# Kernel tuning notes

Hardware: AMD Instinct MI355X
Metric: run time of the kernel (lower is better)

Reference implementation:

```python
import jax, jax.numpy as jnp
import numpy as np

N_NODES = 16384
HID_IN = 1024   # hid_size (GCN in/out dim)
HID_MID = 1500  # hidden_size
N_EDGES = 131072


def setup_inputs() -> dict:
    key = jax.random.key(0)
    k1, k2, k3, k4, k5, k6 = jax.random.split(key, 6)
    x = jax.random.normal(k1, (N_NODES, HID_IN), dtype=jnp.float32)
    edge_index = jax.random.randint(k2, (2, N_EDGES), 0, N_NODES, dtype=jnp.int64)
    # GCNConv weights (glorot-ish scale) and biases
    W1 = jax.random.normal(k3, (HID_IN, HID_MID), dtype=jnp.float32) / np.sqrt(HID_IN)
    b1 = jnp.zeros((HID_MID,), dtype=jnp.float32)
    W2 = jax.random.normal(k4, (HID_MID, HID_IN), dtype=jnp.float32) / np.sqrt(HID_MID)
    b2 = jnp.zeros((HID_IN,), dtype=jnp.float32)
    return {"x": x, "edge_index": edge_index, "W1": W1, "b1": b1, "W2": W2, "b2": b2}


def _gcn_conv(x, W, b, src, dst, inv_sqrt_deg, n_nodes):
    # PyG GCNConv: out[i] = sum_{(j->i)} d_j^{-1/2} d_i^{-1/2} (x W)[j] + b
    h = x @ W                                   # [N, out]
    norm = inv_sqrt_deg[src] * inv_sqrt_deg[dst]  # [E]
    msg = h[src] * norm[:, None]                 # gather + scale [E, out]
    out = jax.ops.segment_sum(msg, dst, num_segments=n_nodes)
    return out + b


def reference(x, edge_index, W1, b1, W2, b2):
    n = x.shape[0]
    # add self-loops (GCNConv default)
    loops = jnp.arange(n, dtype=edge_index.dtype)
    src = jnp.concatenate([edge_index[0], loops])
    dst = jnp.concatenate([edge_index[1], loops])
    deg = jax.ops.segment_sum(jnp.ones_like(dst, dtype=x.dtype), dst, num_segments=n)
    inv_sqrt_deg = jnp.where(deg > 0, jax.lax.rsqrt(jnp.maximum(deg, 1.0)), 0.0)
    h = _gcn_conv(x, W1, b1, src, dst, inv_sqrt_deg, n)
    h = jax.nn.relu(h)  # dropout skipped (eval mode)
    out = _gcn_conv(h, W2, b2, src, dst, inv_sqrt_deg, n)
    return out
```

## Files before the change

kernel.cpp:

```cpp
#include <hip/hip_runtime.h>
#include <cstdint>
#include <cstddef>

#define NN 16384
#define DIN 1024
#define DMID 1500
#define DMIDP 1536
#define NE 131072

typedef __bf16 bf16;
typedef __bf16 bf16x4 __attribute__((ext_vector_type(4)));
typedef __bf16 bf16x8 __attribute__((ext_vector_type(8)));
typedef float f32x4 __attribute__((ext_vector_type(4)));

#define GLOBAL_AS __attribute__((address_space(1)))
#define LDS_AS __attribute__((address_space(3)))

__device__ __forceinline__ void gload_lds16(const bf16* g, bf16* l) {
    __builtin_amdgcn_global_load_lds((GLOBAL_AS const unsigned int*)(g),
                                     (LDS_AS unsigned int*)(l), 16, 0, 0);
}

#define SBAR() asm volatile("s_barrier" ::: "memory")
#define WAITV_(N) asm volatile("s_waitcnt vmcnt(" #N ")" ::: "memory")
#define WAITV(N) WAITV_(N)
#define WAITL0() asm volatile("s_waitcnt lgkmcnt(0)" ::: "memory")

__global__ void k_zero_cnt(int* cnt) {
    cnt[blockIdx.x * 256 + threadIdx.x] = 0;
}

__global__ void k_count(const int* __restrict__ dst, int* cnt) {
    int e = blockIdx.x * 256 + threadIdx.x;
    atomicAdd(&cnt[dst[e]], 1);
}

__global__ __launch_bounds__(1024) void k_scan(const int* __restrict__ cnt,
                                               int* __restrict__ rowptr,
                                               int* __restrict__ cursor,
                                               float* __restrict__ isd) {
    __shared__ int sums[1024];
    int t = threadIdx.x;
    int base = t * 16;
    int v[16], p[16];
    int s = 0;
#pragma unroll
    for (int k = 0; k < 16; ++k) {
        v[k] = cnt[base + k];
        p[k] = (v[k] + 7) & ~7;
        s += p[k];
    }
    sums[t] = s;
    __syncthreads();
    for (int off = 1; off < 1024; off <<= 1) {
        int y = (t >= off) ? sums[t - off] : 0;
        __syncthreads();
        sums[t] += y;
        __syncthreads();
    }
    int run = sums[t] - s;
#pragma unroll
    for (int k = 0; k < 16; ++k) {
        rowptr[base + k] = run;
        cursor[base + k] = run;
        isd[base + k] = rsqrtf((float)(v[k] + 1));
        run += p[k];
    }
    if (t == 1023) rowptr[NN] = run;
}

__global__ void k_fill(const int* __restrict__ src, const int* __restrict__ dst,
                       int* cursor, const float* __restrict__ isd,
                       int* __restrict__ csr_src, float* __restrict__ csr_w) {
    int e = blockIdx.x * 256 + threadIdx.x;
    int s = src[e], d = dst[e];
    int pos = atomicAdd(&cursor[d], 1);
    csr_src[pos] = s;
    csr_w[pos] = isd[s] * isd[d];
}

__global__ void k_pad(const int* __restrict__ cnt, const int* __restrict__ rowptr,
                      int* __restrict__ csr_src, float* __restrict__ csr_w) {
    int i = blockIdx.x * 256 + threadIdx.x;
    int c = cnt[i];
    int p = (c + 7) & ~7;
    int base = rowptr[i];
    for (int q = c; q < p; ++q) {
        csr_src[base + q] = i;
        csr_w[base + q] = 0.0f;
    }
}

__global__ void k_cvt_x(const float4* __restrict__ x, bf16x4* __restrict__ xb) {
    int i = blockIdx.x * 256 + threadIdx.x;
    float4 v = x[i];
    bf16x4 o;
    o[0] = (bf16)v.x; o[1] = (bf16)v.y; o[2] = (bf16)v.z; o[3] = (bf16)v.w;
    xb[i] = o;
}

__global__ void k_cvt_w1(const float* __restrict__ W1, bf16* __restrict__ W1b) {
    int n = blockIdx.x;
    for (int k = threadIdx.x; k < DIN; k += 256)
        W1b[n * DIN + k] = (n < DMID) ? (bf16)W1[(size_t)k * DMID + n] : (bf16)0.0f;
}

__global__ void k_cvt_w2(const float* __restrict__ W2, bf16* __restrict__ W2b) {
    int n = blockIdx.x;
    for (int k = threadIdx.x; k < DMIDP; k += 256)
        W2b[n * DMIDP + k] = (k < DMID) ? (bf16)W2[(size_t)k * DIN + n] : (bf16)0.0f;
}

template <int K, int N, bool RELU_BIAS>
__global__ __launch_bounds__(512, 2) void gemm256(const bf16* __restrict__ A,
                                                  const bf16* __restrict__ Bt,
                                                  bf16* __restrict__ C,
                                                  const float* __restrict__ bias) {
    constexpr int NT = K / 64;
    __shared__ __align__(16) bf16 lds[2][2][256 * 64];
    const int tid = threadIdx.x;
    const int w = tid >> 6;
    const int lane = tid & 63;
    const int bm = blockIdx.x, bn = blockIdx.y;
    const int fr = lane & 15, fq = lane >> 4;
    const int wm = w >> 2;
    const int wn = w & 3;
    const int sx = fr & 7;

    const int lrow = lane >> 3;
    const int lslot = (lane & 7) ^ lrow;
    const bf16* gA = A + (size_t)(bm * 256 + w * 8 + lrow) * K + lslot * 8;
    const bf16* gB = Bt + (size_t)(bn * 256 + w * 8 + lrow) * K + lslot * 8;
    bf16* lA0 = &lds[0][0][0] + w * 512;
    bf16* lB0 = &lds[0][1][0] + w * 512;
    bf16* lA1 = &lds[1][0][0] + w * 512;
    bf16* lB1 = &lds[1][1][0] + w * 512;

    f32x4 acc[8][4];
#pragma unroll
    for (int i = 0; i < 8; ++i)
#pragma unroll
        for (int j = 0; j < 4; ++j) acc[i][j] = {0.f, 0.f, 0.f, 0.f};

#define STAGE(T, LA, LB)                                                  \
    do {                                                                  \
        const bf16* _ga = gA + (size_t)(T) * 64;                          \
        const bf16* _gb = gB + (size_t)(T) * 64;                          \
        _Pragma("unroll") for (int r = 0; r < 4; ++r)                     \
            gload_lds16(_ga + (size_t)r * (64 * K), (LA) + r * 4096);     \
        _Pragma("unroll") for (int r = 0; r < 4; ++r)                     \
            gload_lds16(_gb + (size_t)r * (64 * K), (LB) + r * 4096);     \
    } while (0)

#define LDA4(BUF, MH, KS)                                                             \
    _Pragma("unroll") for (int mt = 0; mt < 4; ++mt) {                                \
        int row = wm * 128 + (MH) * 64 + mt * 16 + fr;                                \
        int sl = (((KS) << 2) | fq) ^ sx;                                             \
        af[mt] = *(const bf16x8*)((const char*)&lds[BUF][0][0] + row * 128 + sl * 16);\
    }
#define LDB4(BUF, KS)                                                                 \
    _Pragma("unroll") for (int nt = 0; nt < 4; ++nt) {                                \
        int row = wn * 64 + nt * 16 + fr;                                             \
        int sl = (((KS) << 2) | fq) ^ sx;                                             \
        bq[nt] = *(const bf16x8*)((const char*)&lds[BUF][1][0] + row * 128 + sl * 16);\
    }
#define MFMA16(MH)                                                                    \
    _Pragma("unroll") for (int mt = 0; mt < 4; ++mt)                                  \
    _Pragma("unroll") for (int nt = 0; nt < 4; ++nt)                                  \
        acc[(MH) * 4 + mt][nt] = __builtin_amdgcn_mfma_f32_16x16x32_bf16(             \
            af[mt], bq[nt], acc[(MH) * 4 + mt][nt], 0, 0, 0);

    STAGE(0, lA0, lB0);
    STAGE(1, lA1, lB1);
    WAITV(8);
    SBAR();

#pragma unroll 2
    for (int t = 0; t < NT; ++t) {
        const int b = t & 1;
        bf16x8 af[4], bq[4];
        LDB4(b, 0); LDA4(b, 0, 0);
        SBAR(); WAITL0();
        __builtin_amdgcn_s_setprio(1); MFMA16(0); __builtin_amdgcn_s_setprio(0);
        SBAR();
        LDA4(b, 1, 0);
        SBAR(); WAITL0();
        __builtin_amdgcn_s_setprio(1); MFMA16(1); __builtin_amdgcn_s_setprio(0);
        SBAR();
        LDB4(b, 1); LDA4(b, 0, 1);
        SBAR(); WAITL0();
        __builtin_amdgcn_s_setprio(1); MFMA16(0); __builtin_amdgcn_s_setprio(0);
        SBAR();
        LDA4(b, 1, 1);
        SBAR(); WAITL0();
        __builtin_amdgcn_s_setprio(1); MFMA16(1); __builtin_amdgcn_s_setprio(0);
        SBAR();
        if (t + 2 < NT) {
            if (b == 0) { STAGE(t + 2, lA0, lB0); } else { STAGE(t + 2, lA1, lB1); }
            WAITV(8);
            SBAR();
        } else if (t + 1 < NT) {
            WAITV(0);
            SBAR();
        }
    }
#undef STAGE
#undef LDA4
#undef LDB4
#undef MFMA16

    float bv[4];
    if (RELU_BIAS) {
#pragma unroll
        for (int nt = 0; nt < 4; ++nt) {
            int col = bn * 256 + wn * 64 + nt * 16 + fr;
            bv[nt] = (col < DMID) ? bias[col] : 0.0f;
        }
    }
#pragma unroll
    for (int mq = 0; mq < 8; ++mq) {
        int row0 = bm * 256 + wm * 128 + mq * 16 + fq * 4;
#pragma unroll
        for (int nt = 0; nt < 4; ++nt) {
            int col = bn * 256 + wn * 64 + nt * 16 + fr;
#pragma unroll
            for (int r = 0; r < 4; ++r) {
                float v = acc[mq][nt][r];
                if (RELU_BIAS) v = fmaxf(v + bv[nt], 0.0f);
                C[(size_t)(row0 + r) * N + col] = (bf16)v;
            }
        }
    }
}

__global__ __launch_bounds__(128) void k_aggX(const bf16* __restrict__ X,
                                              const int* __restrict__ rowptr,
                                              const int* __restrict__ csr_src,
                                              const float* __restrict__ csr_w,
                                              const float* __restrict__ isd,
                                              bf16* __restrict__ XA) {
    int i = blockIdx.x;
    int t = threadIdx.x;
    int c0 = t * 8;
    int beg = rowptr[i], end = rowptr[i + 1];
    float wi = isd[i];
    float w0 = wi * wi;
    float a[8];
    bf16x8 h = *(const bf16x8*)&X[(size_t)i * DIN + c0];
#pragma unroll
    for (int k = 0; k < 8; ++k) a[k] = w0 * (float)h[k];
    for (int e = beg; e < end; e += 8) {
        int j[8];
        float w[8];
        bf16x8 hv[8];
#pragma unroll
        for (int q = 0; q < 8; ++q) { j[q] = csr_src[e + q]; w[q] = csr_w[e + q]; }
#pragma unroll
        for (int q = 0; q < 8; ++q)
            hv[q] = *(const bf16x8*)&X[(size_t)j[q] * DIN + c0];
#pragma unroll
        for (int q = 0; q < 8; ++q)
#pragma unroll
            for (int k = 0; k < 8; ++k) a[k] += w[q] * (float)hv[q][k];
    }
    bf16x8 o;
#pragma unroll
    for (int k = 0; k < 8; ++k) o[k] = (bf16)a[k];
    *(bf16x8*)&XA[(size_t)i * DIN + c0] = o;
}

__global__ __launch_bounds__(128) void k_agg2(const bf16* __restrict__ H,
                                              const int* __restrict__ rowptr,
                                              const int* __restrict__ csr_src,
                                              const float* __restrict__ csr_w,
                                              const float* __restrict__ isd,
                                              const float* __restrict__ b2,
                                              float* __restrict__ out) {
    int i = blockIdx.x;
    int t = threadIdx.x;
    int c0 = t * 8;
    int beg = rowptr[i], end = rowptr[i + 1];
    float wi = isd[i];
    float w0 = wi * wi;
    float a[8];
    bf16x8 h = *(const bf16x8*)&H[(size_t)i * DIN + c0];
#pragma unroll
    for (int k = 0; k < 8; ++k) a[k] = w0 * (float)h[k];
    for (int e = beg; e < end; e += 8) {
        int j[8];
        float w[8];
        bf16x8 hv[8];
#pragma unroll
        for (int q = 0; q < 8; ++q) { j[q] = csr_src[e + q]; w[q] = csr_w[e + q]; }
#pragma unroll
        for (int q = 0; q < 8; ++q)
            hv[q] = *(const bf16x8*)&H[(size_t)j[q] * DIN + c0];
#pragma unroll
        for (int q = 0; q < 8; ++q)
#pragma unroll
            for (int k = 0; k < 8; ++k) a[k] += w[q] * (float)hv[q][k];
    }
    float4 o0, o1;
    o0.x = a[0] + b2[c0 + 0]; o0.y = a[1] + b2[c0 + 1];
    o0.z = a[2] + b2[c0 + 2]; o0.w = a[3] + b2[c0 + 3];
    o1.x = a[4] + b2[c0 + 4]; o1.y = a[5] + b2[c0 + 5];
    o1.z = a[6] + b2[c0 + 6]; o1.w = a[7] + b2[c0 + 7];
    *(float4*)&out[(size_t)i * DIN + c0] = o0;
    *(float4*)&out[(size_t)i * DIN + c0 + 4] = o1;
}

extern "C" void kernel_launch(void* const* d_in, const int* in_sizes, int n_in,
                              void* d_out, int out_size, void* d_ws, size_t ws_size,
                              hipStream_t stream) {
    const float* x = (const float*)d_in[0];
    const int* ei = (const int*)d_in[1];
    const float* W1 = (const float*)d_in[2];
    const float* b1 = (const float*)d_in[3];
    const float* W2 = (const float*)d_in[4];
    const float* b2 = (const float*)d_in[5];
    float* out = (float*)d_out;
    const int* src = ei;
    const int* dst = ei + NE;

    char* ws = (char*)d_ws;
    int* cnt      = (int*)(ws + 0);
    int* cursor   = (int*)(ws + 65536);
    float* isd    = (float*)(ws + 131072);
    int* rowptr   = (int*)(ws + 196608);
    int* csr_src  = (int*)(ws + 327680);
    float* csr_w  = (float*)(ws + 2424832);
    bf16* Xb      = (bf16*)(ws + 4521984);
    bf16* XA      = (bf16*)(ws + 38076416);
    bf16* W1b     = (bf16*)(ws + 71630848);
    bf16* W2b     = (bf16*)(ws + 74776576);
    bf16* Y1b     = (bf16*)(ws + 77922304);
    bf16* H2b     = XA;

    k_zero_cnt<<<NN / 256, 256, 0, stream>>>(cnt);
    k_count<<<NE / 256, 256, 0, stream>>>(dst, cnt);
    k_scan<<<1, 1024, 0, stream>>>(cnt, rowptr, cursor, isd);
    k_fill<<<NE / 256, 256, 0, stream>>>(src, dst, cursor, isd, csr_src, csr_w);
    k_pad<<<NN / 256, 256, 0, stream>>>(cnt, rowptr, csr_src, csr_w);

    k_cvt_x<<<NN * DIN / 4 / 256, 256, 0, stream>>>((const float4*)x, (bf16x4*)Xb);
    k_cvt_w1<<<DMIDP, 256, 0, stream>>>(W1, W1b);
    k_cvt_w2<<<DIN, 256, 0, stream>>>(W2, W2b);

    k_aggX<<<NN, 128, 0, stream>>>(Xb, rowptr, csr_src, csr_w, isd, XA);
    dim3 g1(NN / 256, DMIDP / 256);
    gemm256<DIN, DMIDP, true><<<g1, 512, 0, stream>>>(XA, W1b, Y1b, b1);

    dim3 g2(NN / 256, DIN / 256);
    gemm256<DMIDP, DIN, false><<<g2, 512, 0, stream>>>(Y1b, W2b, H2b, nullptr);
    k_agg2<<<NN, 128, 0, stream>>>(H2b, rowptr, csr_src, csr_w, isd, b2, out);
}
```

Before: 398.2 us.

## Software-pipeline LDS fragment loads with register double buffering in GEMM loop

The GEMM main loop is restructured so LDS-to-register fragment loads for the next MFMA group are issued while the current MFMA group runs. It uses separate a0/a1/b0/b1 register sets, and the next tile's first fragments are prefetched right after the buffer-swap barrier. This drops most of the per-substep barriers and lgkmcnt waits that previously serialized LDS reads and MFMA work. In exchange it uses more VGPRs for fragment buffers and waits on global loads once per iteration. It also removes the unroll-2 pragma, so the buffer index becomes a runtime value.

```diff
diff --git a/kernel.cpp b/kernel.cpp
--- a/kernel.cpp
+++ b/kernel.cpp
@@ -131,10 +131,6 @@
     const int lslot = (lane & 7) ^ lrow;
     const bf16* gA = A + (size_t)(bm * 256 + w * 8 + lrow) * K + lslot * 8;
     const bf16* gB = Bt + (size_t)(bn * 256 + w * 8 + lrow) * K + lslot * 8;
-    bf16* lA0 = &lds[0][0][0] + w * 512;
-    bf16* lB0 = &lds[0][1][0] + w * 512;
-    bf16* lA1 = &lds[1][0][0] + w * 512;
-    bf16* lB1 = &lds[1][1][0] + w * 512;
 
     f32x4 acc[8][4];
 #pragma unroll
@@ -142,67 +138,67 @@
 #pragma unroll
         for (int j = 0; j < 4; ++j) acc[i][j] = {0.f, 0.f, 0.f, 0.f};
 
-#define STAGE(T, LA, LB)                                                  \
-    do {                                                                  \
-        const bf16* _ga = gA + (size_t)(T) * 64;                          \
-        const bf16* _gb = gB + (size_t)(T) * 64;                          \
-        _Pragma("unroll") for (int r = 0; r < 4; ++r)                     \
-            gload_lds16(_ga + (size_t)r * (64 * K), (LA) + r * 4096);     \
-        _Pragma("unroll") for (int r = 0; r < 4; ++r)                     \
-            gload_lds16(_gb + (size_t)r * (64 * K), (LB) + r * 4096);     \
+#define STAGE(T, BUF)                                                          \
+    do {                                                                       \
+        const bf16* _ga = gA + (size_t)(T) * 64;                               \
+        const bf16* _gb = gB + (size_t)(T) * 64;                               \
+        bf16* _la = &lds[BUF][0][0] + w * 512;                                 \
+        bf16* _lb = &lds[BUF][1][0] + w * 512;                                 \
+        _Pragma("unroll") for (int r = 0; r < 4; ++r)                          \
+            gload_lds16(_ga + (size_t)r * (64 * K), _la + r * 4096);           \
+        _Pragma("unroll") for (int r = 0; r < 4; ++r)                          \
+            gload_lds16(_gb + (size_t)r * (64 * K), _lb + r * 4096);           \
     } while (0)
 
-#define LDA4(BUF, MH, KS)                                                             \
-    _Pragma("unroll") for (int mt = 0; mt < 4; ++mt) {                                \
-        int row = wm * 128 + (MH) * 64 + mt * 16 + fr;                                \
-        int sl = (((KS) << 2) | fq) ^ sx;                                             \
-        af[mt] = *(const bf16x8*)((const char*)&lds[BUF][0][0] + row * 128 + sl * 16);\
-    }
-#define LDB4(BUF, KS)                                                                 \
-    _Pragma("unroll") for (int nt = 0; nt < 4; ++nt) {                                \
-        int row = wn * 64 + nt * 16 + fr;                                             \
-        int sl = (((KS) << 2) | fq) ^ sx;                                             \
-        bq[nt] = *(const bf16x8*)((const char*)&lds[BUF][1][0] + row * 128 + sl * 16);\
-    }
-#define MFMA16(MH)                                                                    \
-    _Pragma("unroll") for (int mt = 0; mt < 4; ++mt)                                  \
-    _Pragma("unroll") for (int nt = 0; nt < 4; ++nt)                                  \
-        acc[(MH) * 4 + mt][nt] = __builtin_amdgcn_mfma_f32_16x16x32_bf16(             \
-            af[mt], bq[nt], acc[(MH) * 4 + mt][nt], 0, 0, 0);
-
-    STAGE(0, lA0, lB0);
-    STAGE(1, lA1, lB1);
+#define LDA4(DST, BUF, MH, KS)                                                 \
+    _Pragma("unroll") for (int mt = 0; mt < 4; ++mt) {                         \
+        int row = wm * 128 + (MH) * 64 + mt * 16 + fr;                         \
+        int sl = (((KS) << 2) | fq) ^ sx;                                      \
+        DST[mt] = *(const bf16x8*)((const char*)&lds[BUF][0][0] +              \
+                                   row * 128 + sl * 16);                       \
+    }
+#define LDB4(DST, BUF, KS)                                                     \
+    _Pragma("unroll") for (int nt = 0; nt < 4; ++nt) {                         \
+        int row = wn * 64 + nt * 16 + fr;                                      \
+        int sl = (((KS) << 2) | fq) ^ sx;                                      \
+        DST[nt] = *(const bf16x8*)((const char*)&lds[BUF][1][0] +              \
+                                   row * 128 + sl * 16);                       \
+    }
+#define MFMA16(MH, AF, BF)                                                     \
+    __builtin_amdgcn_s_setprio(1);                                             \
+    _Pragma("unroll") for (int mt = 0; mt < 4; ++mt)                           \
+    _Pragma("unroll") for (int nt = 0; nt < 4; ++nt)                           \
+        acc[(MH) * 4 + mt][nt] = __builtin_amdgcn_mfma_f32_16x16x32_bf16(      \
+            AF[mt], BF[nt], acc[(MH) * 4 + mt][nt], 0, 0, 0);                  \
+    __builtin_amdgcn_s_setprio(0);
+
+    bf16x8 a0[4], a1[4], b0[4], b1[4];
+
+    STAGE(0, 0);
+    STAGE(1, 1);
     WAITV(8);
     SBAR();
-
-#pragma unroll 2
+    LDA4(a0, 0, 0, 0);
+    LDB4(b0, 0, 0);
+
     for (int t = 0; t < NT; ++t) {
         const int b = t & 1;
-        bf16x8 af[4], bq[4];
-        LDB4(b, 0); LDA4(b, 0, 0);
-        SBAR(); WAITL0();
-        __builtin_amdgcn_s_setprio(1); MFMA16(0); __builtin_amdgcn_s_setprio(0);
-        SBAR();
-        LDA4(b, 1, 0);
-        SBAR(); WAITL0();
-        __builtin_amdgcn_s_setprio(1); MFMA16(1); __builtin_amdgcn_s_setprio(0);
-        SBAR();
-        LDB4(b, 1); LDA4(b, 0, 1);
-        SBAR(); WAITL0();
-        __builtin_amdgcn_s_setprio(1); MFMA16(0); __builtin_amdgcn_s_setprio(0);
-        SBAR();
-        LDA4(b, 1, 1);
-        SBAR(); WAITL0();
-        __builtin_amdgcn_s_setprio(1); MFMA16(1); __builtin_amdgcn_s_setprio(0);
-        SBAR();
-        if (t + 2 < NT) {
-            if (b == 0) { STAGE(t + 2, lA0, lB0); } else { STAGE(t + 2, lA1, lB1); }
-            WAITV(8);
-            SBAR();
-        } else if (t + 1 < NT) {
+        LDA4(a1, b, 1, 0);
+        MFMA16(0, a0, b0);
+        LDA4(a0, b, 0, 1);
+        LDB4(b1, b, 1);
+        MFMA16(1, a1, b0);
+        LDA4(a1, b, 1, 1);
+        MFMA16(0, a0, b1);
+        if (t + 1 < NT) {
+            WAITL0();
             WAITV(0);
             SBAR();
+            if (t + 2 < NT) STAGE(t + 2, b);
+            LDA4(a0, b ^ 1, 0, 0);
+            LDB4(b0, b ^ 1, 0);
         }
+        MFMA16(1, a1, b1);
     }
 #undef STAGE
 #undef LDA4
```

Measured after the change: 378.1 us. -5.0%, faster.

## Interleave half-tile global-to-LDS staging with MFMA phases in GEMM main loop

Applied to the files above, without the earlier changes.

Restructures the GEMM main loop so each quarter-phase issues a half-tile of the next A/B stage while computing. A is prefetched one step ahead and B two steps ahead, instead of the whole next tile being staged at the loop end. Register fragments are reorganized so A rows are loaded once per K-half and reused across two B column halves, which cuts LDS reads. This raises register pressure and relies on a subtle buffer-reuse ordering between the A and B buffers.

```diff
diff --git a/kernel.cpp b/kernel.cpp
--- a/kernel.cpp
+++ b/kernel.cpp
@@ -129,12 +129,8 @@
 
     const int lrow = lane >> 3;
     const int lslot = (lane & 7) ^ lrow;
-    const bf16* gA = A + (size_t)(bm * 256 + w * 8 + lrow) * K + lslot * 8;
-    const bf16* gB = Bt + (size_t)(bn * 256 + w * 8 + lrow) * K + lslot * 8;
-    bf16* lA0 = &lds[0][0][0] + w * 512;
-    bf16* lB0 = &lds[0][1][0] + w * 512;
-    bf16* lA1 = &lds[1][0][0] + w * 512;
-    bf16* lB1 = &lds[1][1][0] + w * 512;
+    const bf16* gA = A + (size_t)(bm * 256 + lrow) * K + lslot * 8;
+    const bf16* gB = Bt + (size_t)(bn * 256 + lrow) * K + lslot * 8;
 
     f32x4 acc[8][4];
 #pragma unroll
@@ -142,70 +138,81 @@
 #pragma unroll
         for (int j = 0; j < 4; ++j) acc[i][j] = {0.f, 0.f, 0.f, 0.f};
 
-#define STAGE(T, LA, LB)                                                  \
-    do {                                                                  \
-        const bf16* _ga = gA + (size_t)(T) * 64;                          \
-        const bf16* _gb = gB + (size_t)(T) * 64;                          \
-        _Pragma("unroll") for (int r = 0; r < 4; ++r)                     \
-            gload_lds16(_ga + (size_t)r * (64 * K), (LA) + r * 4096);     \
-        _Pragma("unroll") for (int r = 0; r < 4; ++r)                     \
-            gload_lds16(_gb + (size_t)r * (64 * K), (LB) + r * 4096);     \
+#define STAGEH(T, BUF, MAT, HALF)                                              \
+    do {                                                                       \
+        const bf16* _g = (MAT) ? gB : gA;                                      \
+        bf16* _l = &lds[BUF][MAT][0] + ((HALF) * 128 + w * 16) * 64;           \
+        _Pragma("unroll") for (int r = 0; r < 2; ++r)                          \
+            gload_lds16(_g + (size_t)((HALF) * 128 + w * 16 + r * 8) * K       \
+                           + (size_t)(T) * 64,                                 \
+                        _l + r * 512);                                         \
     } while (0)
 
-#define LDA4(BUF, MH, KS)                                                             \
-    _Pragma("unroll") for (int mt = 0; mt < 4; ++mt) {                                \
-        int row = wm * 128 + (MH) * 64 + mt * 16 + fr;                                \
-        int sl = (((KS) << 2) | fq) ^ sx;                                             \
-        af[mt] = *(const bf16x8*)((const char*)&lds[BUF][0][0] + row * 128 + sl * 16);\
-    }
-#define LDB4(BUF, KS)                                                                 \
-    _Pragma("unroll") for (int nt = 0; nt < 4; ++nt) {                                \
-        int row = wn * 64 + nt * 16 + fr;                                             \
-        int sl = (((KS) << 2) | fq) ^ sx;                                             \
-        bq[nt] = *(const bf16x8*)((const char*)&lds[BUF][1][0] + row * 128 + sl * 16);\
-    }
-#define MFMA16(MH)                                                                    \
-    _Pragma("unroll") for (int mt = 0; mt < 4; ++mt)                                  \
-    _Pragma("unroll") for (int nt = 0; nt < 4; ++nt)                                  \
-        acc[(MH) * 4 + mt][nt] = __builtin_amdgcn_mfma_f32_16x16x32_bf16(             \
-            af[mt], bq[nt], acc[(MH) * 4 + mt][nt], 0, 0, 0);
-
-    STAGE(0, lA0, lB0);
-    STAGE(1, lA1, lB1);
-    WAITV(8);
+#define LDA8(DST, BUF, MH)                                                     \
+    _Pragma("unroll") for (int mt = 0; mt < 4; ++mt)                           \
+    _Pragma("unroll") for (int ks = 0; ks < 2; ++ks) {                         \
+        int row = wm * 128 + (MH) * 64 + mt * 16 + fr;                         \
+        int sl = ((ks << 2) | fq) ^ sx;                                        \
+        DST[mt][ks] = *(const bf16x8*)((const char*)&lds[BUF][0][0] +          \
+                                       row * 128 + sl * 16);                   \
+    }
+#define LDB4(DST, BUF, NH)                                                     \
+    _Pragma("unroll") for (int nt = 0; nt < 2; ++nt)                           \
+    _Pragma("unroll") for (int ks = 0; ks < 2; ++ks) {                         \
+        int row = wn * 64 + (NH) * 32 + nt * 16 + fr;                          \
+        int sl = ((ks << 2) | fq) ^ sx;                                        \
+        DST[nt][ks] = *(const bf16x8*)((const char*)&lds[BUF][1][0] +          \
+                                       row * 128 + sl * 16);                   \
+    }
+#define MFMA16(MH, NH, AF, BF)                                                 \
+    __builtin_amdgcn_s_setprio(1);                                             \
+    _Pragma("unroll") for (int mt = 0; mt < 4; ++mt)                           \
+    _Pragma("unroll") for (int nt = 0; nt < 2; ++nt)                           \
+    _Pragma("unroll") for (int ks = 0; ks < 2; ++ks)                           \
+        acc[(MH) * 4 + mt][(NH) * 2 + nt] =                                    \
+            __builtin_amdgcn_mfma_f32_16x16x32_bf16(                           \
+                AF[mt][ks], BF[nt][ks], acc[(MH) * 4 + mt][(NH) * 2 + nt],     \
+                0, 0, 0);                                                      \
+    __builtin_amdgcn_s_setprio(0);
+
+    STAGEH(0, 0, 0, 0); STAGEH(0, 0, 0, 1);
+    STAGEH(0, 0, 1, 0); STAGEH(0, 0, 1, 1);
+    STAGEH(1, 1, 1, 0); STAGEH(1, 1, 1, 1);
+    WAITV(4);
     SBAR();
 
+    bf16x8 a[4][2], b0[2][2], b1[2][2];
 #pragma unroll 2
     for (int t = 0; t < NT; ++t) {
-        const int b = t & 1;
-        bf16x8 af[4], bq[4];
-        LDB4(b, 0); LDA4(b, 0, 0);
+        const int c = t & 1;
+        LDA8(a, c, 0);
+        LDB4(b0, c, 0);
+        if (t + 1 < NT) STAGEH(t + 1, c ^ 1, 0, 0);
         SBAR(); WAITL0();
-        __builtin_amdgcn_s_setprio(1); MFMA16(0); __builtin_amdgcn_s_setprio(0);
-        SBAR();
-        LDA4(b, 1, 0);
+        MFMA16(0, 0, a, b0);
+        SBAR();
+        LDB4(b1, c, 1);
+        if (t + 1 < NT) STAGEH(t + 1, c ^ 1, 0, 1);
         SBAR(); WAITL0();
-        __builtin_amdgcn_s_setprio(1); MFMA16(1); __builtin_amdgcn_s_setprio(0);
-        SBAR();
-        LDB4(b, 1); LDA4(b, 0, 1);
+        MFMA16(0, 1, a, b1);
+        SBAR();
+        LDA8(a, c, 1);
+        if (t + 2 < NT) STAGEH(t + 2, c, 1, 0);
         SBAR(); WAITL0();
-        __builtin_amdgcn_s_setprio(1); MFMA16(0); __builtin_amdgcn_s_setprio(0);
-        SBAR();
-        LDA4(b, 1, 1);
-        SBAR(); WAITL0();
-        __builtin_amdgcn_s_setprio(1); MFMA16(1); __builtin_amdgcn_s_setprio(0);
+        MFMA16(1, 0, a, b0);
         SBAR();
         if (t + 2 < NT) {
-            if (b == 0) { STAGE(t + 2, lA0, lB0); } else { STAGE(t + 2, lA1, lB1); }
-            WAITV(8);
-            SBAR();
-        } else if (t + 1 < NT) {
+            STAGEH(t + 2, c, 1, 1);
+            WAITV(4);
+        } else {
             WAITV(0);
-            SBAR();
         }
-    }
-#undef STAGE
-#undef LDA4
+        SBAR();
+        MFMA16(1, 1, a, b1);
+        SBAR();
+    }
+#undef STAGEH
+#undef LDA8
 #undef LDB4
 #undef MFMA16
 
```

Measured after the change: 387.7 us. 2.6% less time.
